# Kernel tuning notes

Measured on AMD Instinct MI355X. Metric: run time of the kernel, lower is better.

Reference implementation:

```python
import jax, jax.numpy as jnp
import numpy as np

N_T = 100000   # transaction nodes
N_A = 50000    # account nodes
F = 256        # raw feature dim
H = 256        # hidden_dim
E = 800000     # edges per edge type


def setup_inputs() -> dict:
    key = jax.random.key(0)
    ks = jax.random.split(key, 14)
    s = 1.0 / np.sqrt(F)
    return {
        "x_tx": jax.random.normal(ks[0], (N_T, F), jnp.float32),
        "x_acc": jax.random.normal(ks[1], (N_A, F), jnp.float32),
        "edge_at_src": jax.random.randint(ks[2], (E,), 0, N_A, jnp.int32),
        "edge_at_dst": jax.random.randint(ks[3], (E,), 0, N_T, jnp.int32),
        "edge_ta_src": jax.random.randint(ks[4], (E,), 0, N_T, jnp.int32),
        "edge_ta_dst": jax.random.randint(ks[5], (E,), 0, N_A, jnp.int32),
        "W_l_at": jax.random.normal(ks[6], (F, H), jnp.float32) * s,
        "b_l_at": jnp.zeros((H,), jnp.float32),
        "W_r_at": jax.random.normal(ks[7], (F, H), jnp.float32) * s,
        "W_l_ta": jax.random.normal(ks[8], (F, H), jnp.float32) * s,
        "b_l_ta": jnp.zeros((H,), jnp.float32),
        "W_r_ta": jax.random.normal(ks[9], (F, H), jnp.float32) * s,
        "W_out": jax.random.normal(ks[10], (H, 1), jnp.float32) * (1.0 / np.sqrt(H)),
        "b_out": jnp.zeros((1,), jnp.float32),
    }


def _sage(x_src, x_dst, src_idx, dst_idx, W_l, b_l, W_r, num_dst):
    # PyG SAGEConv (mean aggr): lin_l(mean_j x_src[j]) + lin_r(x_dst)
    msgs = x_src[src_idx]  # [E, F] gather
    summed = jax.ops.segment_sum(msgs, dst_idx, num_segments=num_dst)  # [num_dst, F]
    cnt = jax.ops.segment_sum(jnp.ones((src_idx.shape[0],), x_src.dtype), dst_idx,
                              num_segments=num_dst)
    mean = summed / jnp.maximum(cnt, 1.0)[:, None]  # isolated dst -> zeros
    return mean @ W_l + b_l + x_dst @ W_r


def reference(x_tx, x_acc, edge_at_src, edge_at_dst, edge_ta_src, edge_ta_dst,
              W_l_at, b_l_at, W_r_at, W_l_ta, b_l_ta, W_r_ta, W_out, b_out):
    # account -> transaction SAGEConv
    h_tx = _sage(x_acc, x_tx, edge_at_src, edge_at_dst, W_l_at, b_l_at, W_r_at, N_T)
    # transaction -> account SAGEConv (computed as in HeteroConv, though unused downstream)
    h_acc = _sage(x_tx, x_acc, edge_ta_src, edge_ta_dst, W_l_ta, b_l_ta, W_r_ta, N_A)
    tx_x = jax.nn.relu(h_tx)
    _ = jax.nn.relu(h_acc)
    logits = (tx_x @ W_out + b_out)[:, 0]  # squeeze(-1)
    return logits, tx_x
```

## Files before the change

### kernel.cpp

```cpp
#include <hip/hip_runtime.h>
#include <hip/hip_bf16.h>

typedef __bf16 bf16x8_t __attribute__((ext_vector_type(8)));
typedef __bf16 bf16x4_t __attribute__((ext_vector_type(4)));
typedef float f32x4_t __attribute__((ext_vector_type(4)));

#define M_TX 100000
#define N_AC 50000
#define FDIM 256
#define HDIM 256
#define KTOT 512
#define SCAN_NBLK ((M_TX + 1023) / 1024)

__device__ inline bf16x8_t bzero8() {
    bf16x8_t v;
#pragma unroll
    for (int z = 0; z < 8; ++z) v[z] = (__bf16)0.f;
    return v;
}

__global__ __launch_bounds__(256) void initk3(float* __restrict__ logits,
                                              int* __restrict__ hist,
                                              int* __restrict__ fill,
                                              const float* __restrict__ b_out,
                                              const float* __restrict__ Wl,
                                              const float* __restrict__ Wr,
                                              __bf16* __restrict__ WT) {
    int i = blockIdx.x * 256 + threadIdx.x;
    if (i < M_TX) {
        logits[i] = b_out[0];
        hist[i] = 0;
        fill[i] = 0;
    }
    if (i < FDIM * HDIM) {
        int k = i >> 8;
        int n = i & 255;
        WT[n * KTOT + k]       = (__bf16)Wl[k * HDIM + n];
        WT[n * KTOT + 256 + k] = (__bf16)Wr[k * HDIM + n];
    }
}

__global__ __launch_bounds__(256) void cvt2k(const float* __restrict__ s1,
                                             __bf16* __restrict__ d1, int n4_1,
                                             const float* __restrict__ s2,
                                             __bf16* __restrict__ d2, int n4_2) {
    int stride = gridDim.x * 256;
    int tot = n4_1 + n4_2;
    for (int i = blockIdx.x * 256 + threadIdx.x; i < tot; i += stride) {
        const f32x4_t* sp;
        bf16x4_t* dp;
        if (i < n4_1) { sp = (const f32x4_t*)s1 + i; dp = (bf16x4_t*)d1 + i; }
        else          { sp = (const f32x4_t*)s2 + (i - n4_1); dp = (bf16x4_t*)d2 + (i - n4_1); }
        f32x4_t v = *sp;
        bf16x4_t w;
        w[0] = (__bf16)v.x; w[1] = (__bf16)v.y;
        w[2] = (__bf16)v.z; w[3] = (__bf16)v.w;
        *dp = w;
    }
}

__global__ __launch_bounds__(256) void cvtk(const float* __restrict__ src,
                                            __bf16* __restrict__ dst, int n4) {
    int stride = gridDim.x * 256;
    for (int i = blockIdx.x * 256 + threadIdx.x; i < n4; i += stride) {
        f32x4_t v = ((const f32x4_t*)src)[i];
        bf16x4_t w;
        w[0] = (__bf16)v.x; w[1] = (__bf16)v.y;
        w[2] = (__bf16)v.z; w[3] = (__bf16)v.w;
        ((bf16x4_t*)dst)[i] = w;
    }
}

__global__ __launch_bounds__(256) void histk(const int* __restrict__ edst,
                                             int* __restrict__ hist, int E) {
    int e = blockIdx.x * 256 + threadIdx.x;
    if (e >= E) return;
    atomicAdd(&hist[edst[e]], 1);
}

__global__ __launch_bounds__(1024) void scan1k(const int* __restrict__ hist,
                                               int* __restrict__ row_start,
                                               int* __restrict__ partials) {
    __shared__ int tmp[1024];
    const int b = blockIdx.x;
    const int t = threadIdx.x;
    const int i = b * 1024 + t;
    int v = (i < M_TX) ? hist[i] : 0;
    tmp[t] = v;
    __syncthreads();
    for (int off = 1; off < 1024; off <<= 1) {
        int u = (t >= off) ? tmp[t - off] : 0;
        __syncthreads();
        tmp[t] += u;
        __syncthreads();
    }
    if (i < M_TX) row_start[i] = tmp[t] - v;
    if (t == 1023) partials[b] = tmp[1023];
}

__global__ __launch_bounds__(128) void scan2k(int* __restrict__ partials,
                                              int* __restrict__ row_start) {
    __shared__ int tmp[128];
    const int t = threadIdx.x;
    int v = (t < SCAN_NBLK) ? partials[t] : 0;
    tmp[t] = v;
    __syncthreads();
    for (int off = 1; off < 128; off <<= 1) {
        int u = (t >= off) ? tmp[t - off] : 0;
        __syncthreads();
        tmp[t] += u;
        __syncthreads();
    }
    if (t < SCAN_NBLK) partials[t] = tmp[t] - v;
    if (t == 127) row_start[M_TX] = tmp[127];
}

__global__ __launch_bounds__(1024) void scan3k(int* __restrict__ row_start,
                                               const int* __restrict__ partials) {
    const int i = blockIdx.x * 1024 + threadIdx.x;
    if (i < M_TX) row_start[i] += partials[blockIdx.x];
}

__global__ __launch_bounds__(256) void scatterk(const int* __restrict__ esrc,
                                                const int* __restrict__ edst,
                                                const int* __restrict__ row_start,
                                                int* __restrict__ fill,
                                                int* __restrict__ sorted_src, int E) {
    int e = blockIdx.x * 256 + threadIdx.x;
    if (e >= E) return;
    int d = edst[e];
    int pos = row_start[d] + atomicAdd(&fill[d], 1);
    sorted_src[pos] = esrc[e];
}

__global__ __launch_bounds__(256) void gatherk(const float* __restrict__ x_acc,
                                               const __bf16* __restrict__ xab,
                                               const int* __restrict__ sorted_src,
                                               const int* __restrict__ row_start,
                                               float* __restrict__ summed,
                                               __bf16* __restrict__ meanb) {
    int gw = (blockIdx.x * 256 + threadIdx.x) >> 6;
    if (gw >= M_TX) return;
    int lane = threadIdx.x & 63;
    int start = row_start[gw];
    int end = row_start[gw + 1];
    if (xab && meanb) {
        const int l5 = lane & 31;
        const int half = lane >> 5;
        f32x4_t a0 = {0.f, 0.f, 0.f, 0.f}, a1 = {0.f, 0.f, 0.f, 0.f};
        for (int base = start; base < end; base += 64) {
            int n = end - base; if (n > 64) n = 64;
            int s = 0;
            if (base + lane < end) s = sorted_src[base + lane];
            int np = (n + 1) >> 1;
            for (int j2 = 0; j2 < np; ++j2) {
                int idx = 2 * j2 + half;
                int sj = __shfl(s, idx);
                if (idx < n) {
                    bf16x8_t v = *(const bf16x8_t*)(xab + (long)sj * FDIM + l5 * 8);
                    a0.x += (float)v[0]; a0.y += (float)v[1];
                    a0.z += (float)v[2]; a0.w += (float)v[3];
                    a1.x += (float)v[4]; a1.y += (float)v[5];
                    a1.z += (float)v[6]; a1.w += (float)v[7];
                }
            }
        }
        a0.x += __shfl_xor(a0.x, 32); a0.y += __shfl_xor(a0.y, 32);
        a0.z += __shfl_xor(a0.z, 32); a0.w += __shfl_xor(a0.w, 32);
        a1.x += __shfl_xor(a1.x, 32); a1.y += __shfl_xor(a1.y, 32);
        a1.z += __shfl_xor(a1.z, 32); a1.w += __shfl_xor(a1.w, 32);
        if (half == 0) {
            float inv = 1.0f / fmaxf((float)(end - start), 1.0f);
            bf16x8_t w;
            w[0] = (__bf16)(a0.x * inv); w[1] = (__bf16)(a0.y * inv);
            w[2] = (__bf16)(a0.z * inv); w[3] = (__bf16)(a0.w * inv);
            w[4] = (__bf16)(a1.x * inv); w[5] = (__bf16)(a1.y * inv);
            w[6] = (__bf16)(a1.z * inv); w[7] = (__bf16)(a1.w * inv);
            *(bf16x8_t*)(meanb + (long)gw * FDIM + l5 * 8) = w;
        }
        return;
    }
    f32x4_t acc = {0.f, 0.f, 0.f, 0.f};
    if (xab) {
        for (int base = start; base < end; base += 64) {
            int n = end - base; if (n > 64) n = 64;
            int s = 0;
            if (base + lane < end) s = sorted_src[base + lane];
            for (int j = 0; j < n; ++j) {
                int sj = __shfl(s, j);
                const bf16x4_t v = *(const bf16x4_t*)(xab + (long)sj * FDIM + lane * 4);
                acc.x += (float)v[0]; acc.y += (float)v[1];
                acc.z += (float)v[2]; acc.w += (float)v[3];
            }
        }
    } else {
        for (int base = start; base < end; base += 64) {
            int n = end - base; if (n > 64) n = 64;
            int s = 0;
            if (base + lane < end) s = sorted_src[base + lane];
            for (int j = 0; j < n; ++j) {
                int sj = __shfl(s, j);
                const f32x4_t v = *(const f32x4_t*)(x_acc + (long)sj * FDIM + lane * 4);
                acc.x += v.x; acc.y += v.y; acc.z += v.z; acc.w += v.w;
            }
        }
    }
    if (meanb) {
        float inv = 1.0f / fmaxf((float)(end - start), 1.0f);
        bf16x4_t w;
        w[0] = (__bf16)(acc.x * inv); w[1] = (__bf16)(acc.y * inv);
        w[2] = (__bf16)(acc.z * inv); w[3] = (__bf16)(acc.w * inv);
        *(bf16x4_t*)(meanb + (long)gw * FDIM + lane * 4) = w;
    } else {
        *(f32x4_t*)(summed + (long)gw * FDIM + lane * 4) = acc;
    }
}

__global__ __launch_bounds__(512) void gemmk(const float* __restrict__ x_tx,
                                             const __bf16* __restrict__ xtb,
                                             const float* __restrict__ summed,
                                             const __bf16* __restrict__ meanb,
                                             const int* __restrict__ row_start,
                                             const __bf16* __restrict__ WT,
                                             const float* __restrict__ b_l,
                                             const float* __restrict__ W_out,
                                             float* __restrict__ tx_out,
                                             float* __restrict__ logits) {
    __shared__ __bf16 As[128][72];
    __shared__ __bf16 Bs[256][72];

    const int m0 = blockIdx.x * 128;
    const int tid = threadIdx.x;
    const int wid = tid >> 6;
    const int lane = tid & 63;
    const int wm = wid >> 2;
    const int wn = wid & 3;
    const int lc = lane & 15;
    const int lr = lane >> 4;

    f32x4_t acc[4][4];
#pragma unroll
    for (int i = 0; i < 4; ++i)
#pragma unroll
        for (int j = 0; j < 4; ++j) acc[i][j] = (f32x4_t){0.f, 0.f, 0.f, 0.f};

    const int ar = tid >> 2;
    const int acq = tid & 3;
    const int arm = m0 + ar;
    const bool arow_ok = arm < M_TX;

    if (meanb && xtb) {
        bf16x8_t pa0, pa1, pb[4];
        {
            const __bf16* bb = meanb + (long)arm * FDIM + acq * 16;
            pa0 = bzero8(); pa1 = bzero8();
            if (arow_ok) { pa0 = *(const bf16x8_t*)bb; pa1 = *(const bf16x8_t*)(bb + 8); }
#pragma unroll
            for (int i = 0; i < 4; ++i) {
                int t2 = tid + i * 512;
                pb[i] = *(const bf16x8_t*)(WT + (t2 >> 3) * KTOT + (t2 & 7) * 8);
            }
        }
        for (int kc = 0; kc < 8; ++kc) {
            __syncthreads();
            *(bf16x8_t*)(&As[ar][acq * 16]) = pa0;
            *(bf16x8_t*)(&As[ar][acq * 16 + 8]) = pa1;
#pragma unroll
            for (int i = 0; i < 4; ++i) {
                int t2 = tid + i * 512;
                *(bf16x8_t*)(&Bs[t2 >> 3][(t2 & 7) * 8]) = pb[i];
            }
            __syncthreads();
            if (kc < 7) {
                int kn = kc + 1;
                const __bf16* bsrc = (kn < 4) ? meanb : xtb;
                const __bf16* bb = bsrc + (long)arm * FDIM + ((kn & 3) * 64) + acq * 16;
                pa0 = bzero8(); pa1 = bzero8();
                if (arow_ok) { pa0 = *(const bf16x8_t*)bb; pa1 = *(const bf16x8_t*)(bb + 8); }
#pragma unroll
                for (int i = 0; i < 4; ++i) {
                    int t2 = tid + i * 512;
                    pb[i] = *(const bf16x8_t*)(WT + (t2 >> 3) * KTOT + kn * 64 + (t2 & 7) * 8);
                }
            }
            const int kfr = lr * 8;
#pragma unroll
            for (int kk = 0; kk < 2; ++kk) {
                bf16x8_t af[4], bfr[4];
#pragma unroll
                for (int f = 0; f < 4; ++f) {
                    af[f] = *(const bf16x8_t*)(&As[wm * 64 + f * 16 + lc][kk * 32 + kfr]);
                    bfr[f] = *(const bf16x8_t*)(&Bs[wn * 64 + f * 16 + lc][kk * 32 + kfr]);
                }
#pragma unroll
                for (int fm = 0; fm < 4; ++fm)
#pragma unroll
                    for (int fn = 0; fn < 4; ++fn)
                        acc[fm][fn] = __builtin_amdgcn_mfma_f32_16x16x32_bf16(
                            af[fm], bfr[fn], acc[fm][fn], 0, 0, 0);
            }
        }
    } else {
        float invc = 1.0f;
        {
            int idx = arow_ok ? arm : (M_TX - 1);
            int c = row_start[idx + 1] - row_start[idx];
            invc = 1.0f / fmaxf((float)c, 1.0f);
        }
        for (int kc = 0; kc < 8; ++kc) {
            __syncthreads();
            {
                const bool first = kc < 4;
                const int kb = (kc & 3) * 64;
                const float sc = first ? invc : 1.0f;
                const float* base = first ? (summed + (long)arm * FDIM + kb)
                                          : (x_tx + (long)arm * FDIM + kb);
#pragma unroll
                for (int c4 = 0; c4 < 4; ++c4) {
                    int kk = acq * 16 + c4 * 4;
                    f32x4_t v = {0.f, 0.f, 0.f, 0.f};
                    if (arow_ok) v = *(const f32x4_t*)(base + kk);
                    bf16x4_t w;
                    w[0] = (__bf16)(v.x * sc);
                    w[1] = (__bf16)(v.y * sc);
                    w[2] = (__bf16)(v.z * sc);
                    w[3] = (__bf16)(v.w * sc);
                    *(bf16x4_t*)(&As[ar][kk]) = w;
                }
            }
#pragma unroll
            for (int i = 0; i < 4; ++i) {
                int t2 = tid + i * 512;
                int n = t2 >> 3;
                int c = t2 & 7;
                bf16x8_t v = *(const bf16x8_t*)(WT + n * KTOT + kc * 64 + c * 8);
                *(bf16x8_t*)(&Bs[n][c * 8]) = v;
            }
            __syncthreads();
            const int kfr = lr * 8;
#pragma unroll
            for (int kk = 0; kk < 2; ++kk) {
                bf16x8_t af[4], bfr[4];
#pragma unroll
                for (int f = 0; f < 4; ++f) {
                    af[f] = *(const bf16x8_t*)(&As[wm * 64 + f * 16 + lc][kk * 32 + kfr]);
                    bfr[f] = *(const bf16x8_t*)(&Bs[wn * 64 + f * 16 + lc][kk * 32 + kfr]);
                }
#pragma unroll
                for (int fm = 0; fm < 4; ++fm)
#pragma unroll
                    for (int fn = 0; fn < 4; ++fn)
                        acc[fm][fn] = __builtin_amdgcn_mfma_f32_16x16x32_bf16(
                            af[fm], bfr[fn], acc[fm][fn], 0, 0, 0);
            }
        }
    }

    float wout[4], bl[4];
#pragma unroll
    for (int fn = 0; fn < 4; ++fn) {
        int col = wn * 64 + fn * 16 + lc;
        wout[fn] = W_out[col];
        bl[fn] = b_l[col];
    }
#pragma unroll
    for (int fm = 0; fm < 4; ++fm) {
        float part[4] = {0.f, 0.f, 0.f, 0.f};
#pragma unroll
        for (int fn = 0; fn < 4; ++fn) {
            int col = wn * 64 + fn * 16 + lc;
#pragma unroll
            for (int r = 0; r < 4; ++r) {
                int row = m0 + wm * 64 + fm * 16 + lr * 4 + r;
                float h = acc[fm][fn][r] + bl[fn];
                h = fmaxf(h, 0.0f);
                if (row < M_TX) tx_out[(long)row * HDIM + col] = h;
                part[r] += h * wout[fn];
            }
        }
#pragma unroll
        for (int r = 0; r < 4; ++r) {
            float p = part[r];
            p += __shfl_xor(p, 1);
            p += __shfl_xor(p, 2);
            p += __shfl_xor(p, 4);
            p += __shfl_xor(p, 8);
            int row = m0 + wm * 64 + fm * 16 + lr * 4 + r;
            if (lc == 0 && row < M_TX) unsafeAtomicAdd(logits + row, p);
        }
    }
}

extern "C" void kernel_launch(void* const* d_in, const int* in_sizes, int n_in,
                              void* d_out, int out_size, void* d_ws, size_t ws_size,
                              hipStream_t stream) {
    const float* x_tx  = (const float*)d_in[0];
    const float* x_acc = (const float*)d_in[1];
    const int* e_src   = (const int*)d_in[2];
    const int* e_dst   = (const int*)d_in[3];
    const float* W_l   = (const float*)d_in[6];
    const float* b_l   = (const float*)d_in[7];
    const float* W_r   = (const float*)d_in[8];
    const float* W_out = (const float*)d_in[12];
    const float* b_out = (const float*)d_in[13];

    float* out = (float*)d_out;
    float* logits = out;
    float* summed = out + M_TX;

    char* ws = (char*)d_ws;
    size_t off = 0;
    auto alloc = [&](size_t bytes) {
        size_t o = off;
        off = (off + bytes + 255) & ~(size_t)255;
        return o;
    };
    size_t o_WT       = alloc((size_t)HDIM * KTOT * 2);
    size_t o_rowstart = alloc(((size_t)M_TX + 1) * 4);
    size_t o_fill     = alloc((size_t)M_TX * 4);
    size_t o_sorted   = alloc((size_t)800000 * 4);
    size_t o_hist     = alloc((size_t)M_TX * 4);
    size_t o_part     = alloc((size_t)SCAN_NBLK * 4);
    size_t o_xa       = alloc((size_t)N_AC * FDIM * 2);
    size_t lvlA_end   = off;
    size_t o_mean     = alloc((size_t)M_TX * FDIM * 2);
    size_t lvlB_end   = off;
    size_t o_xt       = alloc((size_t)M_TX * FDIM * 2);
    size_t lvlC_end   = off;

    __bf16* WT       = (__bf16*)(ws + o_WT);
    int* row_start   = (int*)(ws + o_rowstart);
    int* fill        = (int*)(ws + o_fill);
    int* sorted_src  = (int*)(ws + o_sorted);
    int* histp       = (int*)(ws + o_hist);
    int* partials    = (int*)(ws + o_part);

    const bool lvlA = ws_size >= lvlA_end;
    const bool lvlB = ws_size >= lvlB_end;
    const bool lvlC = ws_size >= lvlC_end;
    __bf16* xab   = lvlA ? (__bf16*)(ws + o_xa)   : nullptr;
    __bf16* meanb = lvlB ? (__bf16*)(ws + o_mean) : nullptr;
    __bf16* xtb   = lvlC ? (__bf16*)(ws + o_xt)   : nullptr;

    const int E = in_sizes[2];

    hipLaunchKernelGGL(initk3, dim3((M_TX + 255) / 256), dim3(256), 0, stream,
                       logits, histp, fill, b_out, W_l, W_r, WT);
    if (xab && xtb)
        hipLaunchKernelGGL(cvt2k, dim3(2048), dim3(256), 0, stream,
                           x_acc, xab, N_AC * FDIM / 4, x_tx, xtb, M_TX * FDIM / 4);
    else if (xab)
        hipLaunchKernelGGL(cvtk, dim3(2048), dim3(256), 0, stream,
                           x_acc, xab, N_AC * FDIM / 4);
    hipLaunchKernelGGL(histk, dim3((E + 255) / 256), dim3(256), 0, stream,
                       e_dst, histp, E);
    hipLaunchKernelGGL(scan1k, dim3(SCAN_NBLK), dim3(1024), 0, stream,
                       histp, row_start, partials);
    hipLaunchKernelGGL(scan2k, dim3(1), dim3(128), 0, stream, partials, row_start);
    hipLaunchKernelGGL(scan3k, dim3(SCAN_NBLK), dim3(1024), 0, stream,
                       row_start, partials);
    hipLaunchKernelGGL(scatterk, dim3((E + 255) / 256), dim3(256), 0, stream,
                       e_src, e_dst, row_start, fill, sorted_src, E);
    hipLaunchKernelGGL(gatherk, dim3(M_TX / 4), dim3(256), 0, stream,
                       x_acc, xab, sorted_src, row_start, summed, meanb);
    hipLaunchKernelGGL(gemmk, dim3((M_TX + 127) / 128), dim3(512), 0, stream,
                       x_tx, xtb, summed, meanb, row_start, WT, b_l, W_out,
                       out + M_TX, logits);
}
```

Baseline: 450.5 us.

## Add LDS-free register-direct bf16 MFMA GEMM kernel for the bf16 path

Adds gemmk2, a GEMM kernel that loads A (meanb and xtb) and the weight fragments directly from global memory into registers with no shared-memory staging or barriers. It uses 64-row tiles with four waves, each wave covering 64 output columns. It is launched whenever the bf16 buffers exist; the old LDS kernel stays as the fp32 fallback. This removes LDS traffic and syncs, but each wave now re-reads A rows and WT from global/L2, with strided row accesses that may coalesce poorly.

```diff
diff --git a/kernel.cpp b/kernel.cpp
--- a/kernel.cpp
+++ b/kernel.cpp
@@ -216,10 +216,96 @@
     }
 }
 
+__global__ __launch_bounds__(256) void gemmk2(const __bf16* __restrict__ meanb,
+                                              const __bf16* __restrict__ xtb,
+                                              const __bf16* __restrict__ WT,
+                                              const float* __restrict__ b_l,
+                                              const float* __restrict__ W_out,
+                                              float* __restrict__ tx_out,
+                                              float* __restrict__ logits) {
+    const int tid = threadIdx.x;
+    const int w = tid >> 6;
+    const int lane = tid & 63;
+    const int lc = lane & 15;
+    const int lr = lane >> 4;
+    const long m0 = (long)blockIdx.x * 64;
+
+    f32x4_t acc[4][4];
+#pragma unroll
+    for (int i = 0; i < 4; ++i)
+#pragma unroll
+        for (int j = 0; j < 4; ++j) acc[i][j] = (f32x4_t){0.f, 0.f, 0.f, 0.f};
+
+    long ra[4];
+#pragma unroll
+    for (int f = 0; f < 4; ++f) {
+        long r = m0 + f * 16 + lc;
+        if (r >= M_TX) r = M_TX - 1;
+        ra[f] = r * FDIM;
+    }
+    long rb[4];
+#pragma unroll
+    for (int f = 0; f < 4; ++f) rb[f] = (long)(w * 64 + f * 16 + lc) * KTOT;
+
+    const int kfr = lr * 8;
+#pragma unroll
+    for (int half = 0; half < 2; ++half) {
+        const __bf16* Asrc = half ? xtb : meanb;
+#pragma unroll 2
+        for (int kt = 0; kt < 8; ++kt) {
+            const int ka = kt * 32 + kfr;
+            const int kb = half * 256 + kt * 32 + kfr;
+            bf16x8_t af[4], bfr[4];
+#pragma unroll
+            for (int f = 0; f < 4; ++f) af[f] = *(const bf16x8_t*)(Asrc + ra[f] + ka);
+#pragma unroll
+            for (int f = 0; f < 4; ++f) bfr[f] = *(const bf16x8_t*)(WT + rb[f] + kb);
+#pragma unroll
+            for (int fm = 0; fm < 4; ++fm)
+#pragma unroll
+                for (int fn = 0; fn < 4; ++fn)
+                    acc[fm][fn] = __builtin_amdgcn_mfma_f32_16x16x32_bf16(
+                        af[fm], bfr[fn], acc[fm][fn], 0, 0, 0);
+        }
+    }
+
+    float wout[4], bl[4];
+#pragma unroll
+    for (int fn = 0; fn < 4; ++fn) {
+        int col = w * 64 + fn * 16 + lc;
+        wout[fn] = W_out[col];
+        bl[fn] = b_l[col];
+    }
+#pragma unroll
+    for (int fm = 0; fm < 4; ++fm) {
+        float part[4] = {0.f, 0.f, 0.f, 0.f};
+#pragma unroll
+        for (int fn = 0; fn < 4; ++fn) {
+            int col = w * 64 + fn * 16 + lc;
+#pragma unroll
+            for (int r = 0; r < 4; ++r) {
+                long row = m0 + fm * 16 + lr * 4 + r;
+                float h = acc[fm][fn][r] + bl[fn];
+                h = fmaxf(h, 0.0f);
+                if (row < M_TX) tx_out[row * HDIM + col] = h;
+                part[r] += h * wout[fn];
+            }
+        }
+#pragma unroll
+        for (int r = 0; r < 4; ++r) {
+            float p = part[r];
+            p += __shfl_xor(p, 1);
+            p += __shfl_xor(p, 2);
+            p += __shfl_xor(p, 4);
+            p += __shfl_xor(p, 8);
+            long row = m0 + fm * 16 + lr * 4 + r;
+            if (lc == 0 && row < M_TX) unsafeAtomicAdd(logits + row, p);
+        }
+    }
+}
+
 __global__ __launch_bounds__(512) void gemmk(const float* __restrict__ x_tx,
-                                             const __bf16* __restrict__ xtb,
                                              const float* __restrict__ summed,
-                                             const __bf16* __restrict__ meanb,
                                              const int* __restrict__ row_start,
                                              const __bf16* __restrict__ WT,
                                              const float* __restrict__ b_l,
@@ -248,111 +334,58 @@
     const int acq = tid & 3;
     const int arm = m0 + ar;
     const bool arow_ok = arm < M_TX;
-
-    if (meanb && xtb) {
-        bf16x8_t pa0, pa1, pb[4];
+    float invc;
+    {
+        int idx = arow_ok ? arm : (M_TX - 1);
+        int c = row_start[idx + 1] - row_start[idx];
+        invc = 1.0f / fmaxf((float)c, 1.0f);
+    }
+
+    for (int kc = 0; kc < 8; ++kc) {
+        __syncthreads();
         {
-            const __bf16* bb = meanb + (long)arm * FDIM + acq * 16;
-            pa0 = bzero8(); pa1 = bzero8();
-            if (arow_ok) { pa0 = *(const bf16x8_t*)bb; pa1 = *(const bf16x8_t*)(bb + 8); }
-#pragma unroll
-            for (int i = 0; i < 4; ++i) {
-                int t2 = tid + i * 512;
-                pb[i] = *(const bf16x8_t*)(WT + (t2 >> 3) * KTOT + (t2 & 7) * 8);
-            }
-        }
-        for (int kc = 0; kc < 8; ++kc) {
-            __syncthreads();
-            *(bf16x8_t*)(&As[ar][acq * 16]) = pa0;
-            *(bf16x8_t*)(&As[ar][acq * 16 + 8]) = pa1;
-#pragma unroll
-            for (int i = 0; i < 4; ++i) {
-                int t2 = tid + i * 512;
-                *(bf16x8_t*)(&Bs[t2 >> 3][(t2 & 7) * 8]) = pb[i];
-            }
-            __syncthreads();
-            if (kc < 7) {
-                int kn = kc + 1;
-                const __bf16* bsrc = (kn < 4) ? meanb : xtb;
-                const __bf16* bb = bsrc + (long)arm * FDIM + ((kn & 3) * 64) + acq * 16;
-                pa0 = bzero8(); pa1 = bzero8();
-                if (arow_ok) { pa0 = *(const bf16x8_t*)bb; pa1 = *(const bf16x8_t*)(bb + 8); }
-#pragma unroll
-                for (int i = 0; i < 4; ++i) {
-                    int t2 = tid + i * 512;
-                    pb[i] = *(const bf16x8_t*)(WT + (t2 >> 3) * KTOT + kn * 64 + (t2 & 7) * 8);
-                }
-            }
-            const int kfr = lr * 8;
-#pragma unroll
-            for (int kk = 0; kk < 2; ++kk) {
-                bf16x8_t af[4], bfr[4];
-#pragma unroll
-                for (int f = 0; f < 4; ++f) {
-                    af[f] = *(const bf16x8_t*)(&As[wm * 64 + f * 16 + lc][kk * 32 + kfr]);
-                    bfr[f] = *(const bf16x8_t*)(&Bs[wn * 64 + f * 16 + lc][kk * 32 + kfr]);
-                }
-#pragma unroll
-                for (int fm = 0; fm < 4; ++fm)
-#pragma unroll
-                    for (int fn = 0; fn < 4; ++fn)
-                        acc[fm][fn] = __builtin_amdgcn_mfma_f32_16x16x32_bf16(
-                            af[fm], bfr[fn], acc[fm][fn], 0, 0, 0);
-            }
-        }
-    } else {
-        float invc = 1.0f;
-        {
-            int idx = arow_ok ? arm : (M_TX - 1);
-            int c = row_start[idx + 1] - row_start[idx];
-            invc = 1.0f / fmaxf((float)c, 1.0f);
-        }
-        for (int kc = 0; kc < 8; ++kc) {
-            __syncthreads();
-            {
-                const bool first = kc < 4;
-                const int kb = (kc & 3) * 64;
-                const float sc = first ? invc : 1.0f;
-                const float* base = first ? (summed + (long)arm * FDIM + kb)
-                                          : (x_tx + (long)arm * FDIM + kb);
-#pragma unroll
-                for (int c4 = 0; c4 < 4; ++c4) {
-                    int kk = acq * 16 + c4 * 4;
-                    f32x4_t v = {0.f, 0.f, 0.f, 0.f};
-                    if (arow_ok) v = *(const f32x4_t*)(base + kk);
-                    bf16x4_t w;
-                    w[0] = (__bf16)(v.x * sc);
-                    w[1] = (__bf16)(v.y * sc);
-                    w[2] = (__bf16)(v.z * sc);
-                    w[3] = (__bf16)(v.w * sc);
-                    *(bf16x4_t*)(&As[ar][kk]) = w;
-                }
-            }
-#pragma unroll
-            for (int i = 0; i < 4; ++i) {
-                int t2 = tid + i * 512;
-                int n = t2 >> 3;
-                int c = t2 & 7;
-                bf16x8_t v = *(const bf16x8_t*)(WT + n * KTOT + kc * 64 + c * 8);
-                *(bf16x8_t*)(&Bs[n][c * 8]) = v;
-            }
-            __syncthreads();
-            const int kfr = lr * 8;
-#pragma unroll
-            for (int kk = 0; kk < 2; ++kk) {
-                bf16x8_t af[4], bfr[4];
-#pragma unroll
-                for (int f = 0; f < 4; ++f) {
-                    af[f] = *(const bf16x8_t*)(&As[wm * 64 + f * 16 + lc][kk * 32 + kfr]);
-                    bfr[f] = *(const bf16x8_t*)(&Bs[wn * 64 + f * 16 + lc][kk * 32 + kfr]);
-                }
-#pragma unroll
-                for (int fm = 0; fm < 4; ++fm)
-#pragma unroll
-                    for (int fn = 0; fn < 4; ++fn)
-                        acc[fm][fn] = __builtin_amdgcn_mfma_f32_16x16x32_bf16(
-                            af[fm], bfr[fn], acc[fm][fn], 0, 0, 0);
-            }
+            const bool first = kc < 4;
+            const int kb = (kc & 3) * 64;
+            const float sc = first ? invc : 1.0f;
+            const float* base = first ? (summed + (long)arm * FDIM + kb)
+                                      : (x_tx + (long)arm * FDIM + kb);
+#pragma unroll
+            for (int c4 = 0; c4 < 4; ++c4) {
+                int kk = acq * 16 + c4 * 4;
+                f32x4_t v = {0.f, 0.f, 0.f, 0.f};
+                if (arow_ok) v = *(const f32x4_t*)(base + kk);
+                bf16x4_t w;
+                w[0] = (__bf16)(v.x * sc);
+                w[1] = (__bf16)(v.y * sc);
+                w[2] = (__bf16)(v.z * sc);
+                w[3] = (__bf16)(v.w * sc);
+                *(bf16x4_t*)(&As[ar][kk]) = w;
+            }
+        }
+#pragma unroll
+        for (int i = 0; i < 4; ++i) {
+            int t2 = tid + i * 512;
+            int n = t2 >> 3;
+            int c = t2 & 7;
+            bf16x8_t v = *(const bf16x8_t*)(WT + n * KTOT + kc * 64 + c * 8);
+            *(bf16x8_t*)(&Bs[n][c * 8]) = v;
+        }
+        __syncthreads();
+        const int kfr = lr * 8;
+#pragma unroll
+        for (int kk = 0; kk < 2; ++kk) {
+            bf16x8_t af[4], bfr[4];
+#pragma unroll
+            for (int f = 0; f < 4; ++f) {
+                af[f] = *(const bf16x8_t*)(&As[wm * 64 + f * 16 + lc][kk * 32 + kfr]);
+                bfr[f] = *(const bf16x8_t*)(&Bs[wn * 64 + f * 16 + lc][kk * 32 + kfr]);
+            }
+#pragma unroll
+            for (int fm = 0; fm < 4; ++fm)
+#pragma unroll
+                for (int fn = 0; fn < 4; ++fn)
+                    acc[fm][fn] = __builtin_amdgcn_mfma_f32_16x16x32_bf16(
+                        af[fm], bfr[fn], acc[fm][fn], 0, 0, 0);
         }
     }
 
@@ -463,7 +496,10 @@
                        e_src, e_dst, row_start, fill, sorted_src, E);
     hipLaunchKernelGGL(gatherk, dim3(M_TX / 4), dim3(256), 0, stream,
                        x_acc, xab, sorted_src, row_start, summed, meanb);
-    hipLaunchKernelGGL(gemmk, dim3((M_TX + 127) / 128), dim3(512), 0, stream,
-                       x_tx, xtb, summed, meanb, row_start, WT, b_l, W_out,
-                       out + M_TX, logits);
-}
+    if (meanb && xtb)
+        hipLaunchKernelGGL(gemmk2, dim3((M_TX + 63) / 64), dim3(256), 0, stream,
+                           meanb, xtb, WT, b_l, W_out, out + M_TX, logits);
+    else
+        hipLaunchKernelGGL(gemmk, dim3((M_TX + 127) / 128), dim3(512), 0, stream,
+                           x_tx, summed, row_start, WT, b_l, W_out, out + M_TX, logits);
+}
```

After: 502.6 us. 1.12x slower.
